# Optimization experiments

Measured on AMD Instinct MI355X. Metric: run time of the kernel, lower is better.

Reference implementation:

```python
import jax, jax.numpy as jnp
import numpy as np

N_NODES = 50000
N_EDGES = 800000
HID = 128
NF = 128
EC = 100
IN_DIM = 5
N_BLOCKS = 6
CUTOFF = 10.0
LOG2 = float(np.log(2.0))


def ssp(x):
    # ShiftedSoftplus: softplus(x) - log(2)
    return jax.nn.softplus(x) - LOG2


def setup_inputs() -> dict:
    key = jax.random.key(0)
    ks = jax.random.split(key, 16)
    s = 0.05
    inp = {
        "z": jax.random.normal(ks[0], (N_NODES, IN_DIM + HID), dtype=jnp.float32),
        "edge_index": jax.random.randint(ks[1], (2, N_EDGES), 0, N_NODES, dtype=jnp.int32),
        "edge_length": jax.random.uniform(ks[2], (N_EDGES,), dtype=jnp.float32) * 12.0,
        "edge_attr": jax.random.normal(ks[3], (N_EDGES, EC), dtype=jnp.float32),
        # node embedding linear (input_dim -> hidden)
        "emblin_w": jax.random.normal(ks[4], (IN_DIM, HID), dtype=jnp.float32) * s,
        "emblin_b": jnp.zeros((HID,), dtype=jnp.float32),
        # per-block stacked params [N_BLOCKS, ...]
        "lin1_w": jax.random.normal(ks[5], (N_BLOCKS, HID, NF), dtype=jnp.float32) * s,
        "nn_w1": jax.random.normal(ks[6], (N_BLOCKS, EC, NF), dtype=jnp.float32) * s,
        "nn_b1": jnp.zeros((N_BLOCKS, NF), dtype=jnp.float32),
        "nn_w2": jax.random.normal(ks[7], (N_BLOCKS, NF, NF), dtype=jnp.float32) * s,
        "nn_b2": jnp.zeros((N_BLOCKS, NF), dtype=jnp.float32),
        "lin2_w": jax.random.normal(ks[8], (N_BLOCKS, NF, HID), dtype=jnp.float32) * s,
        "lin2_b": jnp.zeros((N_BLOCKS, HID), dtype=jnp.float32),
        "lin_w": jax.random.normal(ks[9], (N_BLOCKS, HID, HID), dtype=jnp.float32) * s,
        "lin_b": jnp.zeros((N_BLOCKS, HID), dtype=jnp.float32),
    }
    return inp


def reference(z, edge_index, edge_length, edge_attr, emblin_w, emblin_b,
              lin1_w, nn_w1, nn_b1, nn_w2, nn_b2, lin2_w, lin2_b, lin_w, lin_b):
    zf, ptemb = z[:, :IN_DIM], z[:, IN_DIM:]
    h = zf @ emblin_w + emblin_b + ptemb  # [N, HID]
    src, dst = edge_index[0], edge_index[1]
    # hard cutoff mask (smooth=False)
    C = ((edge_length <= CUTOFF) & (edge_length >= 0.0)).astype(h.dtype)[:, None]  # [E,1]
    n = h.shape[0]
    for i in range(N_BLOCKS):
        # edge filter network
        W = ssp(edge_attr @ nn_w1[i] + nn_b1[i]) @ nn_w2[i] + nn_b2[i]  # [E, NF]
        W = W * C
        x = h @ lin1_w[i]  # [N, NF], no bias
        msg = x[src] * W  # gather-multiply  [E, NF]
        agg = jax.ops.segment_sum(msg, dst, num_segments=n)  # scatter-add [N, NF]
        x = agg @ lin2_w[i] + lin2_b[i]
        x = ssp(x)
        x = x @ lin_w[i] + lin_b[i]
        h = h + x
    return h
```

## Files before the change

### kernel.cpp

```cpp
#include <hip/hip_runtime.h>
#include <cstddef>

typedef __bf16 bf16;
typedef bf16 bf16x4 __attribute__((ext_vector_type(4)));
typedef bf16 bf16x8 __attribute__((ext_vector_type(8)));
typedef float f32x4 __attribute__((ext_vector_type(4)));

#define N_NODES 50000
#define N_EDGES 800000
#define HID 128
#define NF 128
#define EC 100
#define NBLK 6
#define IN_DIM 5
#define LN2 0.69314718055994530942f
#define LDST 136
#define MST 136
#define EAS 112
#define FRAG_ELEMS 16384
#define HIST_PAD 50176

__device__ __forceinline__ float ssp_f(float v) {
  float e = __expf(-fabsf(v));
  return fmaxf(v, 0.0f) + __logf(1.0f + e) - LN2;
}

__device__ __forceinline__ f32x4 zero4() {
  f32x4 v; v[0] = 0.f; v[1] = 0.f; v[2] = 0.f; v[3] = 0.f; return v;
}

__global__ void repack_kernel(const float* __restrict__ src, bf16* __restrict__ dst,
                              int K, int srcStride) {
  const int m = blockIdx.x;
  const float* s = src + (size_t)m * srcStride;
  bf16* d = dst + (size_t)m * FRAG_ELEMS;
  const int tid = threadIdx.x;
  const int wave = tid >> 6, lane = tid & 63;
  const int quad = lane >> 4, lanelo = lane & 15;
  const int col = wave * 32 + lanelo;
#pragma unroll
  for (int nt = 0; nt < 2; nt++)
#pragma unroll
    for (int ks = 0; ks < 4; ks++) {
      bf16x8 f;
#pragma unroll
      for (int j = 0; j < 8; j++) {
        int k = ks * 32 + quad * 8 + j;
        f[j] = (bf16)((k < K) ? s[(size_t)k * 128 + col + nt * 16] : 0.0f);
      }
      *(bf16x8*)&d[(size_t)(((wave * 2 + nt) * 4 + ks) * 64 + lane) * 8] = f;
    }
}

__global__ void hist_kernel(const int* __restrict__ ei, const float* __restrict__ elen,
                            int* __restrict__ hist, int* __restrict__ nvalid) {
  int e = blockIdx.x * 256 + threadIdx.x;
  if (e < N_EDGES) {
    float L = elen[e];
    if (L <= 10.0f && L >= 0.0f) {
      atomicAdd(&hist[ei[N_EDGES + e]], 1);
      atomicAdd(nvalid, 1);
    }
  }
}

__global__ void scan_blocks_kernel(const int* __restrict__ in, int* __restrict__ out,
                                   int* __restrict__ bsums) {
  __shared__ int s[256];
  int i = blockIdx.x * 256 + threadIdx.x;
  int v = in[i];
  s[threadIdx.x] = v;
  __syncthreads();
#pragma unroll
  for (int off = 1; off < 256; off <<= 1) {
    int t = (threadIdx.x >= off) ? s[threadIdx.x - off] : 0;
    __syncthreads();
    s[threadIdx.x] += t;
    __syncthreads();
  }
  out[i] = s[threadIdx.x] - v;
  if (threadIdx.x == 255) bsums[blockIdx.x] = s[255];
}

__global__ void scan_bsums_kernel(int* __restrict__ bsums, int nb) {
  __shared__ int s[256];
  int v = (threadIdx.x < nb) ? bsums[threadIdx.x] : 0;
  s[threadIdx.x] = v;
  __syncthreads();
#pragma unroll
  for (int off = 1; off < 256; off <<= 1) {
    int t = (threadIdx.x >= off) ? s[threadIdx.x - off] : 0;
    __syncthreads();
    s[threadIdx.x] += t;
    __syncthreads();
  }
  if (threadIdx.x < nb) bsums[threadIdx.x] = s[threadIdx.x] - v;
}

__global__ void scan_add_kernel(int* __restrict__ out, const int* __restrict__ bsums,
                                int* __restrict__ cursor) {
  int i = blockIdx.x * 256 + threadIdx.x;
  int v = out[i] + bsums[blockIdx.x];
  out[i] = v;
  cursor[i] = v;
}

__global__ void scatter_kernel(const int* __restrict__ ei, const float* __restrict__ elen,
                               int* __restrict__ cursor, int* __restrict__ rank,
                               int2* __restrict__ einfo) {
  int e = blockIdx.x * 256 + threadIdx.x;
  if (e < N_EDGES) {
    float L = elen[e];
    int rk = -1;
    if (L <= 10.0f && L >= 0.0f) {
      int s = ei[e];
      int d = ei[N_EDGES + e];
      rk = atomicAdd(&cursor[d], 1);
      einfo[rk] = make_int2(s, d);
    }
    rank[e] = rk;
  }
}

__global__ void permute_ea_kernel(const float* __restrict__ ea,
                                  const int* __restrict__ rank,
                                  bf16* __restrict__ eas) {
  __shared__ int s_rk[64];
  const int e0 = blockIdx.x * 64;
  const int tid = threadIdx.x;
  if (tid < 64) s_rk[tid] = rank[e0 + tid];
  __syncthreads();
#pragma unroll
  for (int it = 0; it < 4; it++) {
    int u = tid + it * 256;
    if (u < 64 * 14) {
      int r = u / 14, s = u - r * 14;
      int rk = s_rk[r];
      if (rk < 0) continue;
      const float* src = ea + (size_t)(e0 + r) * EC;
      bf16x8 o;
#pragma unroll
      for (int j = 0; j < 8; j++) o[j] = (bf16)0.0f;
      if (s < 12) {
        float4 a = *(const float4*)&src[s * 8];
        float4 b = *(const float4*)&src[s * 8 + 4];
        o[0] = (bf16)a.x; o[1] = (bf16)a.y; o[2] = (bf16)a.z; o[3] = (bf16)a.w;
        o[4] = (bf16)b.x; o[5] = (bf16)b.y; o[6] = (bf16)b.z; o[7] = (bf16)b.w;
      } else if (s == 12) {
        float4 a = *(const float4*)&src[96];
        o[0] = (bf16)a.x; o[1] = (bf16)a.y; o[2] = (bf16)a.z; o[3] = (bf16)a.w;
      }
      *(bf16x8*)&eas[(size_t)rk * EAS + s * 8] = o;
    }
  }
}

__global__ void zero_kernel(float4* __restrict__ p, int n4) {
  int i = blockIdx.x * 256 + threadIdx.x;
  if (i < n4) p[i] = make_float4(0.f, 0.f, 0.f, 0.f);
}

__global__ __launch_bounds__(256, 4)
void embed_xgemm_kernel(const float* __restrict__ z,
                        const float* __restrict__ ew,
                        const float* __restrict__ eb,
                        const bf16* __restrict__ wf,
                        float* __restrict__ h,
                        float* __restrict__ x) {
  __shared__ bf16 sA[64 * LDST];
  const int tid = threadIdx.x;
  const int wave = tid >> 6, lane = tid & 63;
  const int quad = lane >> 4, lanelo = lane & 15;
  const int ncol0 = wave * 32;
  const int row0 = blockIdx.x * 64;

  bf16x8 Bf[2][4];
#pragma unroll
  for (int nt = 0; nt < 2; nt++)
#pragma unroll
    for (int ks = 0; ks < 4; ks++)
      Bf[nt][ks] = *(const bf16x8*)&wf[(size_t)(((wave * 2 + nt) * 4 + ks) * 64 + lane) * 8];

#pragma unroll
  for (int it = 0; it < 8; it++) {
    int idx = tid + it * 256;
    int r = idx >> 5, c4 = idx & 31;
    int grow = row0 + r;
    float hv[4] = {0.f, 0.f, 0.f, 0.f};
    if (grow < N_NODES) {
      const float* zr = z + (size_t)grow * (IN_DIM + HID);
      float zf[IN_DIM];
#pragma unroll
      for (int k = 0; k < IN_DIM; k++) zf[k] = zr[k];
#pragma unroll
      for (int j = 0; j < 4; j++) {
        int c = c4 * 4 + j;
        float acc = eb[c] + zr[IN_DIM + c];
#pragma unroll
        for (int k = 0; k < IN_DIM; k++) acc = fmaf(zf[k], ew[k * HID + c], acc);
        hv[j] = acc;
        h[(size_t)grow * HID + c] = acc;
      }
    }
    bf16x4 o; o[0] = (bf16)hv[0]; o[1] = (bf16)hv[1]; o[2] = (bf16)hv[2]; o[3] = (bf16)hv[3];
    *(bf16x4*)&sA[r * LDST + c4 * 4] = o;
  }
  __syncthreads();

  f32x4 acc[4][2];
#pragma unroll
  for (int mt = 0; mt < 4; mt++)
#pragma unroll
    for (int nt = 0; nt < 2; nt++) acc[mt][nt] = zero4();
#pragma unroll
  for (int ks = 0; ks < 4; ks++) {
    bf16x8 a[4];
#pragma unroll
    for (int mt = 0; mt < 4; mt++)
      a[mt] = *(const bf16x8*)&sA[(mt * 16 + lanelo) * LDST + ks * 32 + quad * 8];
#pragma unroll
    for (int mt = 0; mt < 4; mt++)
#pragma unroll
      for (int nt = 0; nt < 2; nt++)
        acc[mt][nt] = __builtin_amdgcn_mfma_f32_16x16x32_bf16(a[mt], Bf[nt][ks], acc[mt][nt], 0, 0, 0);
  }
#pragma unroll
  for (int mt = 0; mt < 4; mt++)
#pragma unroll
    for (int r = 0; r < 4; r++) {
      int grow = row0 + mt * 16 + quad * 4 + r;
      if (grow < N_NODES) {
#pragma unroll
        for (int nt = 0; nt < 2; nt++)
          x[(size_t)grow * NF + ncol0 + nt * 16 + lanelo] = acc[mt][nt][r];
      }
    }
}

__global__ __launch_bounds__(256, 4)
void edge_kernel(const bf16* __restrict__ eas,
                 const int2* __restrict__ einfo,
                 const int* __restrict__ nvalid,
                 const bf16* __restrict__ w1f, const float* __restrict__ b1,
                 const bf16* __restrict__ w2f, const float* __restrict__ b2,
                 const float* __restrict__ x,
                 float* __restrict__ agg) {
  __shared__ alignas(16) char s_buf[64 * MST * 4];
  bf16* sA = (bf16*)s_buf;
  float* s_msg = (float*)s_buf;
  __shared__ int s_dst[64];

  const int nv = *nvalid;
  const int e0 = blockIdx.x * 64;
  if (e0 >= nv) return;

  const int tid = threadIdx.x;
  const int wave = tid >> 6, lane = tid & 63;
  const int quad = lane >> 4, lanelo = lane & 15;
  const int ncol0 = wave * 32;

  float xg[4][4][2];
  bool vld[4][4];
#pragma unroll
  for (int mt = 0; mt < 4; mt++)
#pragma unroll
    for (int r = 0; r < 4; r++) {
      int row = mt * 16 + quad * 4 + r;
      int2 sd = einfo[e0 + row];
      bool v = (e0 + row) < nv;
      vld[mt][r] = v;
#pragma unroll
      for (int nt = 0; nt < 2; nt++) {
        float g = x[(size_t)sd.x * NF + ncol0 + nt * 16 + lanelo];
        xg[mt][r][nt] = v ? g : 0.0f;
      }
    }

  bf16x8 Bf1[2][4], Bf2[2][4];
#pragma unroll
  for (int nt = 0; nt < 2; nt++)
#pragma unroll
    for (int ks = 0; ks < 4; ks++) {
      size_t fo = (size_t)(((wave * 2 + nt) * 4 + ks) * 64 + lane) * 8;
      Bf1[nt][ks] = *(const bf16x8*)&w1f[fo];
      Bf2[nt][ks] = *(const bf16x8*)&w2f[fo];
    }
  float bias1[2], bias2[2];
#pragma unroll
  for (int nt = 0; nt < 2; nt++) {
    bias1[nt] = b1[ncol0 + nt * 16 + lanelo];
    bias2[nt] = b2[ncol0 + nt * 16 + lanelo];
  }

#pragma unroll
  for (int it = 0; it < 5; it++) {
    int u = tid + it * 256;
    if (u < 64 * 17) {
      int r = u / 17, s = u - r * 17;
      bf16x8 o;
      if (s < 14 && (e0 + r) < nv) {
        o = *(const bf16x8*)&eas[(size_t)(e0 + r) * EAS + s * 8];
      } else {
#pragma unroll
        for (int j = 0; j < 8; j++) o[j] = (bf16)0.0f;
      }
      *(bf16x8*)&sA[r * LDST + s * 8] = o;
    }
  }
  if (tid < 64) s_dst[tid] = einfo[e0 + tid].y;
  __syncthreads();

  f32x4 acc[4][2];
#pragma unroll
  for (int mt = 0; mt < 4; mt++)
#pragma unroll
    for (int nt = 0; nt < 2; nt++) acc[mt][nt] = zero4();
#pragma unroll
  for (int ks = 0; ks < 4; ks++) {
    bf16x8 a[4];
#pragma unroll
    for (int mt = 0; mt < 4; mt++)
      a[mt] = *(const bf16x8*)&sA[(mt * 16 + lanelo) * LDST + ks * 32 + quad * 8];
#pragma unroll
    for (int mt = 0; mt < 4; mt++)
#pragma unroll
      for (int nt = 0; nt < 2; nt++)
        acc[mt][nt] = __builtin_amdgcn_mfma_f32_16x16x32_bf16(a[mt], Bf1[nt][ks], acc[mt][nt], 0, 0, 0);
  }
  __syncthreads();

#pragma unroll
  for (int mt = 0; mt < 4; mt++)
#pragma unroll
    for (int nt = 0; nt < 2; nt++)
#pragma unroll
      for (int r = 0; r < 4; r++) {
        float v = ssp_f(acc[mt][nt][r] + bias1[nt]);
        sA[(mt * 16 + quad * 4 + r) * LDST + ncol0 + nt * 16 + lanelo] = (bf16)v;
      }
  __syncthreads();

#pragma unroll
  for (int mt = 0; mt < 4; mt++)
#pragma unroll
    for (int nt = 0; nt < 2; nt++) acc[mt][nt] = zero4();
#pragma unroll
  for (int ks = 0; ks < 4; ks++) {
    bf16x8 a[4];
#pragma unroll
    for (int mt = 0; mt < 4; mt++)
      a[mt] = *(const bf16x8*)&sA[(mt * 16 + lanelo) * LDST + ks * 32 + quad * 8];
#pragma unroll
    for (int mt = 0; mt < 4; mt++)
#pragma unroll
      for (int nt = 0; nt < 2; nt++)
        acc[mt][nt] = __builtin_amdgcn_mfma_f32_16x16x32_bf16(a[mt], Bf2[nt][ks], acc[mt][nt], 0, 0, 0);
  }
  __syncthreads();

#pragma unroll
  for (int mt = 0; mt < 4; mt++)
#pragma unroll
    for (int r = 0; r < 4; r++) {
      int row = mt * 16 + quad * 4 + r;
#pragma unroll
      for (int nt = 0; nt < 2; nt++) {
        int col = ncol0 + nt * 16 + lanelo;
        float wv = acc[mt][nt][r] + bias2[nt];
        s_msg[row * MST + col] = vld[mt][r] ? wv * xg[mt][r][nt] : 0.0f;
      }
    }
  __syncthreads();

  {
    const int col = tid & 127;
    const int r0 = (tid >> 7) * 32;
    float acc2 = 0.0f;
    int prev = s_dst[r0];
    for (int r = r0; r < r0 + 32; r++) {
      int d = s_dst[r];
      if (d != prev) {
        atomicAdd(&agg[(size_t)prev * NF + col], acc2);
        acc2 = 0.0f;
        prev = d;
      }
      acc2 += s_msg[r * MST + col];
    }
    atomicAdd(&agg[(size_t)prev * NF + col], acc2);
  }
}

__global__ __launch_bounds__(256, 4)
void node_kernel(const float* __restrict__ agg,
                 const bf16* __restrict__ w1f, const float* __restrict__ b1,
                 const bf16* __restrict__ w2f, const float* __restrict__ b2,
                 const bf16* __restrict__ wxf,
                 float* __restrict__ h,
                 float* __restrict__ x) {
  __shared__ bf16 sA[64 * LDST];
  const int tid = threadIdx.x;
  const int wave = tid >> 6, lane = tid & 63;
  const int quad = lane >> 4, lanelo = lane & 15;
  const int ncol0 = wave * 32;
  const int row0 = blockIdx.x * 64;

  bf16x8 Bf1[2][4], Bf2[2][4];
#pragma unroll
  for (int nt = 0; nt < 2; nt++)
#pragma unroll
    for (int ks = 0; ks < 4; ks++) {
      size_t fo = (size_t)(((wave * 2 + nt) * 4 + ks) * 64 + lane) * 8;
      Bf1[nt][ks] = *(const bf16x8*)&w1f[fo];
      Bf2[nt][ks] = *(const bf16x8*)&w2f[fo];
    }
  float bias1[2], bias2[2];
#pragma unroll
  for (int nt = 0; nt < 2; nt++) {
    bias1[nt] = b1[ncol0 + nt * 16 + lanelo];
    bias2[nt] = b2[ncol0 + nt * 16 + lanelo];
  }

#pragma unroll
  for (int it = 0; it < 8; it++) {
    int idx = tid + it * 256;
    int r = idx >> 5, c4 = idx & 31;
    int grow = row0 + r;
    float4 v = (grow < N_NODES) ? *(const float4*)&agg[(size_t)grow * NF + c4 * 4]
                                : make_float4(0.f, 0.f, 0.f, 0.f);
    bf16x4 o; o[0] = (bf16)v.x; o[1] = (bf16)v.y; o[2] = (bf16)v.z; o[3] = (bf16)v.w;
    *(bf16x4*)&sA[r * LDST + c4 * 4] = o;
  }
  __syncthreads();

  f32x4 acc[4][2];
#pragma unroll
  for (int mt = 0; mt < 4; mt++)
#pragma unroll
    for (int nt = 0; nt < 2; nt++) acc[mt][nt] = zero4();
#pragma unroll
  for (int ks = 0; ks < 4; ks++) {
    bf16x8 a[4];
#pragma unroll
    for (int mt = 0; mt < 4; mt++)
      a[mt] = *(const bf16x8*)&sA[(mt * 16 + lanelo) * LDST + ks * 32 + quad * 8];
#pragma unroll
    for (int mt = 0; mt < 4; mt++)
#pragma unroll
      for (int nt = 0; nt < 2; nt++)
        acc[mt][nt] = __builtin_amdgcn_mfma_f32_16x16x32_bf16(a[mt], Bf1[nt][ks], acc[mt][nt], 0, 0, 0);
  }
  __syncthreads();

#pragma unroll
  for (int mt = 0; mt < 4; mt++)
#pragma unroll
    for (int nt = 0; nt < 2; nt++)
#pragma unroll
      for (int r = 0; r < 4; r++) {
        float v = ssp_f(acc[mt][nt][r] + bias1[nt]);
        sA[(mt * 16 + quad * 4 + r) * LDST + ncol0 + nt * 16 + lanelo] = (bf16)v;
      }
  __syncthreads();

#pragma unroll
  for (int mt = 0; mt < 4; mt++)
#pragma unroll
    for (int nt = 0; nt < 2; nt++) acc[mt][nt] = zero4();
#pragma unroll
  for (int ks = 0; ks < 4; ks++) {
    bf16x8 a[4];
#pragma unroll
    for (int mt = 0; mt < 4; mt++)
      a[mt] = *(const bf16x8*)&sA[(mt * 16 + lanelo) * LDST + ks * 32 + quad * 8];
#pragma unroll
    for (int mt = 0; mt < 4; mt++)
#pragma unroll
      for (int nt = 0; nt < 2; nt++)
        acc[mt][nt] = __builtin_amdgcn_mfma_f32_16x16x32_bf16(a[mt], Bf2[nt][ks], acc[mt][nt], 0, 0, 0);
  }
  __syncthreads();

#pragma unroll
  for (int mt = 0; mt < 4; mt++)
#pragma unroll
    for (int nt = 0; nt < 2; nt++)
#pragma unroll
      for (int r = 0; r < 4; r++) {
        int row = mt * 16 + quad * 4 + r;
        int grow = row0 + row;
        int col = ncol0 + nt * 16 + lanelo;
        float hv = acc[mt][nt][r] + bias2[nt];
        if (grow < N_NODES) {
          size_t off = (size_t)grow * HID + col;
          hv += h[off];
          h[off] = hv;
        }
        sA[row * LDST + col] = (bf16)hv;
      }

  if (wxf != nullptr) {
    bf16x8 Bfx[2][4];
#pragma unroll
    for (int nt = 0; nt < 2; nt++)
#pragma unroll
      for (int ks = 0; ks < 4; ks++)
        Bfx[nt][ks] = *(const bf16x8*)&wxf[(size_t)(((wave * 2 + nt) * 4 + ks) * 64 + lane) * 8];
    __syncthreads();
#pragma unroll
    for (int mt = 0; mt < 4; mt++)
#pragma unroll
      for (int nt = 0; nt < 2; nt++) acc[mt][nt] = zero4();
#pragma unroll
    for (int ks = 0; ks < 4; ks++) {
      bf16x8 a[4];
#pragma unroll
      for (int mt = 0; mt < 4; mt++)
        a[mt] = *(const bf16x8*)&sA[(mt * 16 + lanelo) * LDST + ks * 32 + quad * 8];
#pragma unroll
      for (int mt = 0; mt < 4; mt++)
#pragma unroll
        for (int nt = 0; nt < 2; nt++)
          acc[mt][nt] = __builtin_amdgcn_mfma_f32_16x16x32_bf16(a[mt], Bfx[nt][ks], acc[mt][nt], 0, 0, 0);
    }
#pragma unroll
    for (int mt = 0; mt < 4; mt++)
#pragma unroll
      for (int r = 0; r < 4; r++) {
        int grow = row0 + mt * 16 + quad * 4 + r;
        if (grow < N_NODES) {
#pragma unroll
          for (int nt = 0; nt < 2; nt++)
            x[(size_t)grow * NF + ncol0 + nt * 16 + lanelo] = acc[mt][nt][r];
        }
      }
  }
}

extern "C" void kernel_launch(void* const* d_in, const int* in_sizes, int n_in,
                              void* d_out, int out_size, void* d_ws, size_t ws_size,
                              hipStream_t stream) {
  const float* z        = (const float*)d_in[0];
  const int*   ei       = (const int*)d_in[1];
  const float* elen     = (const float*)d_in[2];
  const float* ea       = (const float*)d_in[3];
  const float* emblin_w = (const float*)d_in[4];
  const float* emblin_b = (const float*)d_in[5];
  const float* lin1_w   = (const float*)d_in[6];
  const float* nn_w1    = (const float*)d_in[7];
  const float* nn_b1    = (const float*)d_in[8];
  const float* nn_w2    = (const float*)d_in[9];
  const float* nn_b2    = (const float*)d_in[10];
  const float* lin2_w   = (const float*)d_in[11];
  const float* lin2_b   = (const float*)d_in[12];
  const float* lin_w    = (const float*)d_in[13];
  const float* lin_b    = (const float*)d_in[14];

  float* h   = (float*)d_out;
  char* base = (char*)d_ws;
  float* x    = (float*)base;  base += (size_t)N_NODES * NF * 4;
  float* agg  = (float*)base;  base += (size_t)N_NODES * NF * 4;
  bf16* wp    = (bf16*)base;   base += (size_t)5 * NBLK * FRAG_ELEMS * 2;
  int* hist   = (int*)base;    base += (size_t)HIST_PAD * 4;
  int* cursor = (int*)base;    base += (size_t)HIST_PAD * 4;
  int* bsums  = (int*)base;    base += 1024;
  int* nvalid = (int*)base;    base += 16;
  int* rank   = (int*)base;    base += (size_t)N_EDGES * 4;
  int2* einfo = (int2*)base;   base += (size_t)N_EDGES * 8;
  bf16* eas   = (bf16*)base;   base += (size_t)N_EDGES * EAS * 2;

  bf16* wp_lin1 = wp;
  bf16* wp_nw1  = wp + 1 * (size_t)NBLK * FRAG_ELEMS;
  bf16* wp_nw2  = wp + 2 * (size_t)NBLK * FRAG_ELEMS;
  bf16* wp_l2   = wp + 3 * (size_t)NBLK * FRAG_ELEMS;
  bf16* wp_l    = wp + 4 * (size_t)NBLK * FRAG_ELEMS;

  repack_kernel<<<NBLK, 256, 0, stream>>>(lin1_w, wp_lin1, HID, HID * NF);
  repack_kernel<<<NBLK, 256, 0, stream>>>(nn_w1, wp_nw1, EC, EC * NF);
  repack_kernel<<<NBLK, 256, 0, stream>>>(nn_w2, wp_nw2, NF, NF * NF);
  repack_kernel<<<NBLK, 256, 0, stream>>>(lin2_w, wp_l2, NF, NF * HID);
  repack_kernel<<<NBLK, 256, 0, stream>>>(lin_w, wp_l, HID, HID * HID);

  const int nb = HIST_PAD / 256;
  zero_kernel<<<(HIST_PAD / 4 + 255) / 256, 256, 0, stream>>>((float4*)hist, HIST_PAD / 4);
  zero_kernel<<<1, 256, 0, stream>>>((float4*)nvalid, 1);
  zero_kernel<<<(N_EDGES * 2 / 4 + 255) / 256, 256, 0, stream>>>((float4*)einfo, N_EDGES * 2 / 4);
  hist_kernel<<<(N_EDGES + 255) / 256, 256, 0, stream>>>(ei, elen, hist, nvalid);
  scan_blocks_kernel<<<nb, 256, 0, stream>>>(hist, hist, bsums);
  scan_bsums_kernel<<<1, 256, 0, stream>>>(bsums, nb);
  scan_add_kernel<<<nb, 256, 0, stream>>>(hist, bsums, cursor);
  scatter_kernel<<<(N_EDGES + 255) / 256, 256, 0, stream>>>(ei, elen, cursor, rank, einfo);
  permute_ea_kernel<<<N_EDGES / 64, 256, 0, stream>>>(ea, rank, eas);

  const int node_tiles = (N_NODES + 63) / 64;
  const int edge_tiles = N_EDGES / 64;

  embed_xgemm_kernel<<<node_tiles, 256, 0, stream>>>(z, emblin_w, emblin_b, wp_lin1, h, x);

  for (int i = 0; i < NBLK; i++) {
    zero_kernel<<<(N_NODES * NF / 4 + 255) / 256, 256, 0, stream>>>((float4*)agg, N_NODES * NF / 4);
    edge_kernel<<<edge_tiles, 256, 0, stream>>>(eas, einfo, nvalid,
        wp_nw1 + (size_t)i * FRAG_ELEMS, nn_b1 + (size_t)i * NF,
        wp_nw2 + (size_t)i * FRAG_ELEMS, nn_b2 + (size_t)i * NF,
        x, agg);
    node_kernel<<<node_tiles, 256, 0, stream>>>(agg,
        wp_l2 + (size_t)i * FRAG_ELEMS, lin2_b + (size_t)i * HID,
        wp_l + (size_t)i * FRAG_ELEMS, lin_b + (size_t)i * HID,
        (i + 1 < NBLK) ? (wp_lin1 + (size_t)(i + 1) * FRAG_ELEMS) : nullptr,
        h, x);
  }
}
```

Before: 1.964 ms.

## Restructure edge kernel segment reduction in registers and fuse agg zeroing

The edge kernel no longer stages messages in a float shared buffer for a per-column scan. Each tile's destination segments are found once with a wave ballot, and messages are reduced directly from MFMA accumulators using cross-lane shuffles before the atomics. The first-layer weight fragments are loaded on the fly, and the second-layer weights and gathered x values are loaded later to cut register pressure and shared memory. The per-block zero kernel is removed: node_kernel now clears agg after reading it. The risks are the serial per-segment loop with many masked adds and the extra global writes in node_kernel.

```diff
diff --git a/kernel.cpp b/kernel.cpp
--- a/kernel.cpp
+++ b/kernel.cpp
@@ -15,7 +15,6 @@
 #define IN_DIM 5
 #define LN2 0.69314718055994530942f
 #define LDST 136
-#define MST 136
 #define EAS 112
 #define FRAG_ELEMS 16384
 #define HIST_PAD 50176
@@ -245,10 +244,11 @@
                  const bf16* __restrict__ w2f, const float* __restrict__ b2,
                  const float* __restrict__ x,
                  float* __restrict__ agg) {
-  __shared__ alignas(16) char s_buf[64 * MST * 4];
-  bf16* sA = (bf16*)s_buf;
-  float* s_msg = (float*)s_buf;
-  __shared__ int s_dst[64];
+  __shared__ bf16 sA[64 * LDST];
+  __shared__ int s_src[64];
+  __shared__ int s_segstart[65];
+  __shared__ int s_segdst[64];
+  __shared__ int s_nseg;
 
   const int nv = *nvalid;
   const int e0 = blockIdx.x * 64;
@@ -259,32 +259,6 @@
   const int quad = lane >> 4, lanelo = lane & 15;
   const int ncol0 = wave * 32;
 
-  float xg[4][4][2];
-  bool vld[4][4];
-#pragma unroll
-  for (int mt = 0; mt < 4; mt++)
-#pragma unroll
-    for (int r = 0; r < 4; r++) {
-      int row = mt * 16 + quad * 4 + r;
-      int2 sd = einfo[e0 + row];
-      bool v = (e0 + row) < nv;
-      vld[mt][r] = v;
-#pragma unroll
-      for (int nt = 0; nt < 2; nt++) {
-        float g = x[(size_t)sd.x * NF + ncol0 + nt * 16 + lanelo];
-        xg[mt][r][nt] = v ? g : 0.0f;
-      }
-    }
-
-  bf16x8 Bf1[2][4], Bf2[2][4];
-#pragma unroll
-  for (int nt = 0; nt < 2; nt++)
-#pragma unroll
-    for (int ks = 0; ks < 4; ks++) {
-      size_t fo = (size_t)(((wave * 2 + nt) * 4 + ks) * 64 + lane) * 8;
-      Bf1[nt][ks] = *(const bf16x8*)&w1f[fo];
-      Bf2[nt][ks] = *(const bf16x8*)&w2f[fo];
-    }
   float bias1[2], bias2[2];
 #pragma unroll
   for (int nt = 0; nt < 2; nt++) {
@@ -307,7 +281,20 @@
       *(bf16x8*)&sA[r * LDST + s * 8] = o;
     }
   }
-  if (tid < 64) s_dst[tid] = einfo[e0 + tid].y;
+  if (wave == 0) {
+    int2 sd = einfo[e0 + lane];
+    s_src[lane] = sd.x;
+    int prevd = __shfl_up(sd.y, 1);
+    bool flag = (lane == 0) || (sd.y != prevd);
+    unsigned long long bm = __ballot(flag);
+    int segid = __popcll(bm & ((1ull << lane) - 1));
+    if (flag) { s_segstart[segid] = lane; s_segdst[segid] = sd.y; }
+    if (lane == 0) {
+      int ns = __popcll(bm);
+      s_nseg = ns;
+      s_segstart[ns] = 64;
+    }
+  }
   __syncthreads();
 
   f32x4 acc[4][2];
@@ -321,13 +308,40 @@
 #pragma unroll
     for (int mt = 0; mt < 4; mt++)
       a[mt] = *(const bf16x8*)&sA[(mt * 16 + lanelo) * LDST + ks * 32 + quad * 8];
-#pragma unroll
-    for (int mt = 0; mt < 4; mt++)
-#pragma unroll
-      for (int nt = 0; nt < 2; nt++)
-        acc[mt][nt] = __builtin_amdgcn_mfma_f32_16x16x32_bf16(a[mt], Bf1[nt][ks], acc[mt][nt], 0, 0, 0);
-  }
-  __syncthreads();
+    bf16x8 bf1;
+#pragma unroll
+    for (int mt = 0; mt < 4; mt++) {
+      if (mt == 0) {  }
+      bf1 = *(const bf16x8*)&w1f[(size_t)(((wave * 2 + 0) * 4 + ks) * 64 + lane) * 8];
+      acc[mt][0] = __builtin_amdgcn_mfma_f32_16x16x32_bf16(a[mt], bf1, acc[mt][0], 0, 0, 0);
+      bf1 = *(const bf16x8*)&w1f[(size_t)(((wave * 2 + 1) * 4 + ks) * 64 + lane) * 8];
+      acc[mt][1] = __builtin_amdgcn_mfma_f32_16x16x32_bf16(a[mt], bf1, acc[mt][1], 0, 0, 0);
+    }
+  }
+  __syncthreads();
+
+  f32x4 Bf2r[2][4];
+#pragma unroll
+  for (int nt = 0; nt < 2; nt++)
+#pragma unroll
+    for (int ks = 0; ks < 4; ks++) {
+      Bf2r[nt][ks] = *(const f32x4*)&w2f[(size_t)(((wave * 2 + nt) * 4 + ks) * 64 + lane) * 8];
+      asm volatile("" : "+v"(Bf2r[nt][ks]));
+    }
+
+  float xg[4][4][2];
+#pragma unroll
+  for (int mt = 0; mt < 4; mt++)
+#pragma unroll
+    for (int r = 0; r < 4; r++) {
+      int row = mt * 16 + quad * 4 + r;
+      int srcn = s_src[row];
+#pragma unroll
+      for (int nt = 0; nt < 2; nt++) {
+        xg[mt][r][nt] = x[(size_t)srcn * NF + ncol0 + nt * 16 + lanelo];
+        asm volatile("" : "+v"(xg[mt][r][nt]));
+      }
+    }
 
 #pragma unroll
   for (int mt = 0; mt < 4; mt++)
@@ -354,44 +368,47 @@
     for (int mt = 0; mt < 4; mt++)
 #pragma unroll
       for (int nt = 0; nt < 2; nt++)
-        acc[mt][nt] = __builtin_amdgcn_mfma_f32_16x16x32_bf16(a[mt], Bf2[nt][ks], acc[mt][nt], 0, 0, 0);
-  }
-  __syncthreads();
+        acc[mt][nt] = __builtin_amdgcn_mfma_f32_16x16x32_bf16(
+            a[mt], __builtin_bit_cast(bf16x8, Bf2r[nt][ks]), acc[mt][nt], 0, 0, 0);
+  }
 
 #pragma unroll
   for (int mt = 0; mt < 4; mt++)
 #pragma unroll
     for (int r = 0; r < 4; r++) {
       int row = mt * 16 + quad * 4 + r;
+      bool valid = (e0 + row) < nv;
 #pragma unroll
       for (int nt = 0; nt < 2; nt++) {
-        int col = ncol0 + nt * 16 + lanelo;
         float wv = acc[mt][nt][r] + bias2[nt];
-        s_msg[row * MST + col] = vld[mt][r] ? wv * xg[mt][r][nt] : 0.0f;
-      }
-    }
-  __syncthreads();
-
-  {
-    const int col = tid & 127;
-    const int r0 = (tid >> 7) * 32;
-    float acc2 = 0.0f;
-    int prev = s_dst[r0];
-    for (int r = r0; r < r0 + 32; r++) {
-      int d = s_dst[r];
-      if (d != prev) {
-        atomicAdd(&agg[(size_t)prev * NF + col], acc2);
-        acc2 = 0.0f;
-        prev = d;
-      }
-      acc2 += s_msg[r * MST + col];
-    }
-    atomicAdd(&agg[(size_t)prev * NF + col], acc2);
+        acc[mt][nt][r] = valid ? wv * xg[mt][r][nt] : 0.0f;
+      }
+    }
+
+  const int nseg = s_nseg;
+  for (int s = 0; s < nseg; ++s) {
+    const int lo = s_segstart[s], hi = s_segstart[s + 1];
+    const int dd = s_segdst[s];
+    float v0 = 0.f, v1 = 0.f;
+#pragma unroll
+    for (int k = 0; k < 16; ++k) {
+      const int mt = k >> 2, r = k & 3;
+      int row = mt * 16 + quad * 4 + r;
+      bool in = (row >= lo) && (row < hi);
+      v0 += in ? acc[mt][0][r] : 0.f;
+      v1 += in ? acc[mt][1][r] : 0.f;
+    }
+    v0 += __shfl_xor(v0, 16); v0 += __shfl_xor(v0, 32);
+    v1 += __shfl_xor(v1, 16); v1 += __shfl_xor(v1, 32);
+    if (quad == 0) {
+      atomicAdd(&agg[(size_t)dd * NF + ncol0 + lanelo], v0);
+      atomicAdd(&agg[(size_t)dd * NF + ncol0 + 16 + lanelo], v1);
+    }
   }
 }
 
 __global__ __launch_bounds__(256, 4)
-void node_kernel(const float* __restrict__ agg,
+void node_kernel(float* __restrict__ agg,
                  const bf16* __restrict__ w1f, const float* __restrict__ b1,
                  const bf16* __restrict__ w2f, const float* __restrict__ b2,
                  const bf16* __restrict__ wxf,
@@ -425,8 +442,11 @@
     int idx = tid + it * 256;
     int r = idx >> 5, c4 = idx & 31;
     int grow = row0 + r;
-    float4 v = (grow < N_NODES) ? *(const float4*)&agg[(size_t)grow * NF + c4 * 4]
-                                : make_float4(0.f, 0.f, 0.f, 0.f);
+    float4 v = make_float4(0.f, 0.f, 0.f, 0.f);
+    if (grow < N_NODES) {
+      v = *(const float4*)&agg[(size_t)grow * NF + c4 * 4];
+      *(float4*)&agg[(size_t)grow * NF + c4 * 4] = make_float4(0.f, 0.f, 0.f, 0.f);
+    }
     bf16x4 o; o[0] = (bf16)v.x; o[1] = (bf16)v.y; o[2] = (bf16)v.z; o[3] = (bf16)v.w;
     *(bf16x4*)&sA[r * LDST + c4 * 4] = o;
   }
@@ -594,10 +614,10 @@
   const int node_tiles = (N_NODES + 63) / 64;
   const int edge_tiles = N_EDGES / 64;
 
+  zero_kernel<<<(N_NODES * NF / 4 + 255) / 256, 256, 0, stream>>>((float4*)agg, N_NODES * NF / 4);
   embed_xgemm_kernel<<<node_tiles, 256, 0, stream>>>(z, emblin_w, emblin_b, wp_lin1, h, x);
 
   for (int i = 0; i < NBLK; i++) {
-    zero_kernel<<<(N_NODES * NF / 4 + 255) / 256, 256, 0, stream>>>((float4*)agg, N_NODES * NF / 4);
     edge_kernel<<<edge_tiles, 256, 0, stream>>>(eas, einfo, nvalid,
         wp_nw1 + (size_t)i * FRAG_ELEMS, nn_b1 + (size_t)i * NF,
         wp_nw2 + (size_t)i * FRAG_ELEMS, nn_b2 + (size_t)i * NF,
```

Measured after the change: 2.303 ms. 17.3% more time.
